# Performance work log

Measured on AMD Instinct MI355X. Metric: run time of the kernel, lower is better.

Reference implementation:

```python
import jax, jax.numpy as jnp
import numpy as np

D_MODEL = 1024
NUM_HEADS = 16
DEPTH = D_MODEL // NUM_HEADS


def setup_inputs() -> dict:
    key = jax.random.key(0)
    ks = jax.random.split(key, 8)
    B, S, D = 2, 2048, D_MODEL
    s = 1.0 / np.sqrt(D)
    return {
        "q": jax.random.normal(ks[0], (B, S, D), jnp.float32),
        "k": jax.random.normal(ks[1], (B, S, D), jnp.float32),
        "v": jax.random.normal(ks[2], (B, S, D), jnp.float32),
        "Wq": jax.random.normal(ks[3], (D, D), jnp.float32) * s,
        "bq": jnp.zeros((D,), jnp.float32),
        "Wk": jax.random.normal(ks[4], (D, D), jnp.float32) * s,
        "bk": jnp.zeros((D,), jnp.float32),
        "Wv": jax.random.normal(ks[5], (D, D), jnp.float32) * s,
        "bv": jnp.zeros((D,), jnp.float32),
        "Wo": jax.random.normal(ks[6], (D, D), jnp.float32) * s,
        "bo": jnp.zeros((D,), jnp.float32),
    }


def _split_heads(x):
    # [B,S,D] -> [B,H,S,depth]
    B, S, _ = x.shape
    return x.reshape(B, S, NUM_HEADS, DEPTH).transpose(0, 2, 1, 3)


def reference(q, k, v, Wq, bq, Wk, bk, Wv, bv, Wo, bo):
    qh = _split_heads(q @ Wq + bq)  # [B,H,S,d]
    kh = _split_heads(k @ Wk + bk)
    vh = _split_heads(v @ Wv + bv)
    scale = 1.0 / jnp.sqrt(jnp.float32(DEPTH))
    logits = jnp.einsum("bhqd,bhkd->bhqk", qh, kh) * scale  # [B,H,S,S]
    weights = jax.nn.softmax(logits, axis=-1)
    attn = jnp.einsum("bhqk,bhkd->bhqd", weights, vh)
    B, H, S, d = attn.shape
    attn = attn.transpose(0, 2, 1, 3).reshape(B, S, H * d)  # [B,S,D]
    return attn @ Wo + bo
```

## Files before the change

### kernel.cpp

```cpp
#include <hip/hip_runtime.h>
#include <hip/hip_bf16.h>
#include <stdint.h>


typedef __attribute__((ext_vector_type(8))) short bf16x8;
typedef __attribute__((ext_vector_type(4))) float f32x4;

#define MFMA16(a, b, c) __builtin_amdgcn_mfma_f32_16x16x32_bf16((a), (b), (c), 0, 0, 0)
#define EXP2(x) __builtin_amdgcn_exp2f(x)

static constexpr int S_LEN = 2048;
static constexpr int DM    = 1024;
static constexpr int DEPTH = 64;
static constexpr float QSCALE = 0.125f * 1.44269504088896340736f;

__device__ __forceinline__ unsigned short f2b(float f) {
  unsigned u = __float_as_uint(f);
  unsigned r = 0x7FFFu + ((u >> 16) & 1u);
  return (unsigned short)((u + r) >> 16);
}

__device__ __forceinline__ unsigned short b16(float f) {
  __hip_bfloat16 h = __float2bfloat16(f);
  union { __hip_bfloat16 h; unsigned short u; } c; c.h = h; return c.u;
}

__device__ __forceinline__ void gload16(const void* g, void* l) {
  __builtin_amdgcn_global_load_lds(
      (const __attribute__((address_space(1))) void*)g,
      (__attribute__((address_space(3))) void*)l, 16, 0, 0);
}

__device__ __forceinline__ void wave_lds_fence() {
  asm volatile("" ::: "memory");
  __builtin_amdgcn_sched_barrier(0);
}

__global__ __launch_bounds__(256) void prep_k(
    const float* __restrict__ xq, const float* __restrict__ xk,
    const float* __restrict__ xv, unsigned short* __restrict__ Xb,
    const float* __restrict__ Wq, const float* __restrict__ Wk,
    const float* __restrict__ Wv, const float* __restrict__ Wo,
    unsigned short* __restrict__ Wt) {
  __shared__ unsigned short ts[64][68];
  const int bid = blockIdx.x;
  const int tid = threadIdx.x;
  if (bid < 6144) {
    const int which = bid >> 11;
    const int xb = bid & 2047;
    const float* X = (which == 0) ? xq : (which == 1) ? xk : xv;
    size_t gid = ((size_t)xb * 256 + tid) * 8;
    float4 v0 = *(const float4*)&X[gid];
    float4 v1 = *(const float4*)&X[gid + 4];
    union { unsigned short u[8]; bf16x8 v; } pk;
    pk.u[0] = f2b(v0.x); pk.u[1] = f2b(v0.y); pk.u[2] = f2b(v0.z); pk.u[3] = f2b(v0.w);
    pk.u[4] = f2b(v1.x); pk.u[5] = f2b(v1.y); pk.u[6] = f2b(v1.z); pk.u[7] = f2b(v1.w);
    *(bf16x8*)&Xb[(size_t)which * 4096 * DM + gid] = pk.v;
    return;
  }
  const int wb = bid - 6144;
  const int w = wb >> 8, tile = wb & 255;
  const int tr = tile >> 4, tc = tile & 15;
  const float* W = (w == 0) ? Wq : (w == 1) ? Wk : (w == 2) ? Wv : Wo;
  unsigned short* T = Wt + (size_t)w * DM * DM;
  const int kr = tid >> 4, nc = (tid & 15) * 4;
  #pragma unroll
  for (int j = 0; j < 4; ++j) {
    int k = tr * 64 + kr + j * 16;
    float4 v = *(const float4*)&W[(size_t)k * DM + tc * 64 + nc];
    ushort4 u; u.x = f2b(v.x); u.y = f2b(v.y); u.z = f2b(v.z); u.w = f2b(v.w);
    *(ushort4*)&ts[kr + j * 16][nc] = u;
  }
  __syncthreads();
  const int nr = tid >> 4, kc = (tid & 15) * 4;
  #pragma unroll
  for (int j = 0; j < 4; ++j) {
    int n = tc * 64 + nr + j * 16;
    ushort4 u;
    u.x = ts[kc + 0][nr + j * 16];
    u.y = ts[kc + 1][nr + j * 16];
    u.z = ts[kc + 2][nr + j * 16];
    u.w = ts[kc + 3][nr + j * 16];
    *(ushort4*)&T[(size_t)n * DM + tr * 64 + kc] = u;
  }
}

__global__ __launch_bounds__(256, 4) void proj_qkv_k(
    const unsigned short* __restrict__ Xb, const unsigned short* __restrict__ Wt,
    const float* __restrict__ bq, const float* __restrict__ bk, const float* __restrict__ bv,
    unsigned short* __restrict__ Qh, unsigned short* __restrict__ Kh,
    unsigned short* __restrict__ Vt) {
  __shared__ __align__(16) unsigned short As[2][128][32];
  __shared__ __align__(16) unsigned short Bs[2][128][32];

  const int z = blockIdx.z;
  const unsigned short* A  = Xb + (size_t)z * 4096 * DM;
  const unsigned short* Bt = Wt + (size_t)z * DM * DM;
  const float* bias = (z == 0) ? bq : (z == 1) ? bk : bv;
  const float scale = (z == 0) ? QSCALE : 1.0f;
  unsigned short* O = (z == 0) ? Qh : (z == 1) ? Kh : Vt;

  const int bm = blockIdx.x, bn = blockIdx.y;
  const int tid = threadIdx.x;
  const int wave = tid >> 6, lane = tid & 63;
  const int wr = wave >> 1, wc = wave & 1;
  const int g = lane >> 4, i16 = lane & 15;
  const int srow = tid >> 2, sslot = tid & 3;

  f32x4 acc[4][4] = {};

  auto stage = [&](int ks, int buf) {
    #pragma unroll
    for (int rnd = 0; rnd < 2; ++rnd) {
      int row = rnd * 64 + srow;
      int sw = sslot ^ ((row >> 1) & 3);
      gload16(&A[(size_t)(bm * 128 + row) * DM + ks * 32 + sw * 8],
              &As[buf][row][sslot * 8]);
      gload16(&Bt[(size_t)(bn * 128 + row) * DM + ks * 32 + sw * 8],
              &Bs[buf][row][sslot * 8]);
    }
  };
  auto compute = [&](int buf) {
    bf16x8 a[4], b[4];
    #pragma unroll
    for (int m = 0; m < 4; ++m) {
      int row = wr * 64 + m * 16 + i16;
      int sl = g ^ ((row >> 1) & 3);
      a[m] = *(const bf16x8*)&As[buf][row][sl * 8];
    }
    #pragma unroll
    for (int n = 0; n < 4; ++n) {
      int row = wc * 64 + n * 16 + i16;
      int sl = g ^ ((row >> 1) & 3);
      b[n] = *(const bf16x8*)&Bs[buf][row][sl * 8];
    }
    #pragma unroll
    for (int m = 0; m < 4; ++m)
      #pragma unroll
      for (int n = 0; n < 4; ++n)
        acc[m][n] = MFMA16(a[m], b[n], acc[m][n]);
  };

  stage(0, 0);
  __syncthreads();
  int cur = 0;
  #pragma unroll 1
  for (int ks = 0; ks < DM / 32; ++ks) {
    if (ks + 1 < DM / 32) stage(ks + 1, cur ^ 1);
    compute(cur);
    __syncthreads();
    cur ^= 1;
  }

  #pragma unroll
  for (int m = 0; m < 4; ++m) {
    #pragma unroll
    for (int n = 0; n < 4; ++n) {
      #pragma unroll
      for (int r = 0; r < 4; ++r) {
        int row = bm * 128 + wr * 64 + m * 16 + g * 4 + r;
        int col = bn * 128 + wc * 64 + n * 16 + i16;
        float v = (acc[m][n][r] + bias[col]) * scale;
        int b_ = row >> 11, s = row & 2047;
        int h = col >> 6, dd = col & 63;
        if (z != 2)
          O[(((size_t)(b_ * 16 + h)) * S_LEN + s) * DEPTH + dd] = f2b(v);
        else
          O[(((size_t)(b_ * 16 + h)) * DEPTH + dd) * S_LEN + s] = f2b(v);
      }
    }
  }
}

__global__ __launch_bounds__(256, 4) void out_proj_k(
    const unsigned short* __restrict__ At, const unsigned short* __restrict__ Wto,
    const float* __restrict__ bo, float* __restrict__ out) {
  __shared__ __align__(16) unsigned short As[2][64][32];
  __shared__ __align__(16) unsigned short Bs[2][128][32];

  const int bm = blockIdx.x, bn = blockIdx.y;
  const int tid = threadIdx.x;
  const int wave = tid >> 6, lane = tid & 63;
  const int wr = wave >> 1, wc = wave & 1;
  const int g = lane >> 4, i16 = lane & 15;
  const int srow = tid >> 2, sslot = tid & 3;

  f32x4 acc[2][4] = {};

  auto stage = [&](int ks, int buf) {
    {
      int sw = sslot ^ ((srow >> 1) & 3);
      gload16(&At[(size_t)(bm * 64 + srow) * DM + ks * 32 + sw * 8],
              &As[buf][srow][sslot * 8]);
    }
    #pragma unroll
    for (int rnd = 0; rnd < 2; ++rnd) {
      int row = rnd * 64 + srow;
      int sw = sslot ^ ((row >> 1) & 3);
      gload16(&Wto[(size_t)(bn * 128 + row) * DM + ks * 32 + sw * 8],
              &Bs[buf][row][sslot * 8]);
    }
  };
  auto compute = [&](int buf) {
    bf16x8 a[2], b[4];
    #pragma unroll
    for (int m = 0; m < 2; ++m) {
      int row = wr * 32 + m * 16 + i16;
      int sl = g ^ ((row >> 1) & 3);
      a[m] = *(const bf16x8*)&As[buf][row][sl * 8];
    }
    #pragma unroll
    for (int n = 0; n < 4; ++n) {
      int row = wc * 64 + n * 16 + i16;
      int sl = g ^ ((row >> 1) & 3);
      b[n] = *(const bf16x8*)&Bs[buf][row][sl * 8];
    }
    #pragma unroll
    for (int m = 0; m < 2; ++m)
      #pragma unroll
      for (int n = 0; n < 4; ++n)
        acc[m][n] = MFMA16(a[m], b[n], acc[m][n]);
  };

  stage(0, 0);
  __syncthreads();
  int cur = 0;
  #pragma unroll 1
  for (int ks = 0; ks < DM / 32; ++ks) {
    if (ks + 1 < DM / 32) stage(ks + 1, cur ^ 1);
    compute(cur);
    __syncthreads();
    cur ^= 1;
  }

  #pragma unroll
  for (int m = 0; m < 2; ++m) {
    #pragma unroll
    for (int n = 0; n < 4; ++n) {
      #pragma unroll
      for (int r = 0; r < 4; ++r) {
        int row = bm * 64 + wr * 32 + m * 16 + g * 4 + r;
        int col = bn * 128 + wc * 64 + n * 16 + i16;
        out[(size_t)row * DM + col] = acc[m][n][r] + bo[col];
      }
    }
  }
}

__global__ __launch_bounds__(256) void attn_k(
    const unsigned short* __restrict__ Qh, const unsigned short* __restrict__ Kh,
    const unsigned short* __restrict__ Vt, unsigned short* __restrict__ Ob) {
  __shared__ unsigned short kv_lds[2][2][64][64];
  __shared__ unsigned short p_lds[4][16][64];

  const int linear = blockIdx.y * 32 + blockIdx.x;
  const int wg = (linear & 7) * 128 + (linear >> 3);
  const int qt = wg & 31, bh = wg >> 5;

  const int tid = threadIdx.x;
  const int wave = tid >> 6, lane = tid & 63;
  const int g = lane >> 4, i16 = lane & 15;

  const unsigned short* Q = Qh + (size_t)bh * S_LEN * DEPTH;
  const unsigned short* K = Kh + (size_t)bh * S_LEN * DEPTH;
  const unsigned short* V = Vt + (size_t)bh * DEPTH * S_LEN;

  const int sr0 = tid >> 3;
  const int ss0 = tid & 7;

  const int qbase = qt * 64 + wave * 16;
  const bf16x8 qa0 = *(const bf16x8*)&Q[(size_t)(qbase + i16) * DEPTH + g * 8];
  const bf16x8 qa1 = *(const bf16x8*)&Q[(size_t)(qbase + i16) * DEPTH + 32 + g * 8];

  const short one_b = (short)0x3F80;
  const bf16x8 ones = {one_b, one_b, one_b, one_b, one_b, one_b, one_b, one_b};

  f32x4 l_acc = {0.f, 0.f, 0.f, 0.f};
  f32x4 o[4] = {};

  #pragma unroll
  for (int j = 0; j < 2; ++j) {
    int r = j * 32 + sr0;
    int sw = ss0 ^ (r & 7);
    gload16(&K[(size_t)r * DEPTH + sw * 8], &kv_lds[0][0][r][ss0 * 8]);
    gload16(&V[(size_t)r * S_LEN + sw * 8], &kv_lds[0][1][r][ss0 * 8]);
  }
  __syncthreads();

  int cur = 0;
  #pragma unroll 1
  for (int t64 = 0; t64 < 32; ++t64) {
    const int kv0 = t64 * 64;
    if (t64 + 1 < 32) {
      const int nkv = kv0 + 64;
      #pragma unroll
      for (int j = 0; j < 2; ++j) {
        int r = j * 32 + sr0;
        int sw = ss0 ^ (r & 7);
        gload16(&K[(size_t)(nkv + r) * DEPTH + sw * 8], &kv_lds[cur ^ 1][0][r][ss0 * 8]);
        gload16(&V[(size_t)r * S_LEN + nkv + sw * 8],   &kv_lds[cur ^ 1][1][r][ss0 * 8]);
      }
    }

    f32x4 sT[4];
    const f32x4 zero = {0.f, 0.f, 0.f, 0.f};
    __builtin_amdgcn_s_setprio(1);
    #pragma unroll
    for (int t = 0; t < 4; ++t) {
      int row = t * 16 + i16;
      int x = row & 7;
      bf16x8 k0 = *(const bf16x8*)&kv_lds[cur][0][row][(g ^ x) * 8];
      bf16x8 k1 = *(const bf16x8*)&kv_lds[cur][0][row][((4 + g) ^ x) * 8];
      f32x4 s = MFMA16(k0, qa0, zero);
      sT[t] = MFMA16(k1, qa1, s);
    }
    __builtin_amdgcn_s_setprio(0);

    bf16x8 vf0[4], vf1[4];
    #pragma unroll
    for (int dt = 0; dt < 4; ++dt) {
      int row = dt * 16 + i16;
      int x = row & 7;
      vf0[dt] = *(const bf16x8*)&kv_lds[cur][1][row][(g ^ x) * 8];
      vf1[dt] = *(const bf16x8*)&kv_lds[cur][1][row][((4 + g) ^ x) * 8];
    }

    #pragma unroll
    for (int t = 0; t < 4; ++t) {
      ushort4 w;
      w.x = b16(EXP2(sT[t][0]));
      w.y = b16(EXP2(sT[t][1]));
      w.z = b16(EXP2(sT[t][2]));
      w.w = b16(EXP2(sT[t][3]));
      int idx = (((t * 2 + (g >> 1)) ^ (i16 & 7)) * 8) + (g & 1) * 4;
      *(ushort4*)&p_lds[wave][i16][idx] = w;
    }
    wave_lds_fence();
    bf16x8 pa0 = *(const bf16x8*)&p_lds[wave][i16][(g ^ (i16 & 7)) * 8];
    bf16x8 pa1 = *(const bf16x8*)&p_lds[wave][i16][((4 + g) ^ (i16 & 7)) * 8];

    __builtin_amdgcn_s_setprio(1);
    #pragma unroll
    for (int dt = 0; dt < 4; ++dt) {
      o[dt] = MFMA16(pa0, vf0[dt], o[dt]);
      o[dt] = MFMA16(pa1, vf1[dt], o[dt]);
    }
    l_acc = MFMA16(pa0, ones, l_acc);
    l_acc = MFMA16(pa1, ones, l_acc);
    __builtin_amdgcn_s_setprio(0);

    __syncthreads();
    cur ^= 1;
  }

  const int b_ = bh >> 4, h = bh & 15;
  f32x4 rinv;
  #pragma unroll
  for (int r = 0; r < 4; ++r)
    rinv[r] = 1.0f / l_acc[r];
  #pragma unroll
  for (int dt = 0; dt < 4; ++dt) {
    #pragma unroll
    for (int r = 0; r < 4; ++r) {
      int qrow = qbase + g * 4 + r;
      float val = o[dt][r] * rinv[r];
      Ob[((size_t)(b_ * S_LEN + qrow)) * DM + h * DEPTH + dt * 16 + i16] = f2b(val);
    }
  }
}

extern "C" void kernel_launch(void* const* d_in, const int* in_sizes, int n_in,
                              void* d_out, int out_size, void* d_ws, size_t ws_size,
                              hipStream_t stream) {
  const float* q  = (const float*)d_in[0];
  const float* k  = (const float*)d_in[1];
  const float* v  = (const float*)d_in[2];
  const float* Wq = (const float*)d_in[3];
  const float* bq = (const float*)d_in[4];
  const float* Wk = (const float*)d_in[5];
  const float* bk = (const float*)d_in[6];
  const float* Wv = (const float*)d_in[7];
  const float* bv = (const float*)d_in[8];
  const float* Wo = (const float*)d_in[9];
  const float* bo = (const float*)d_in[10];
  float* out = (float*)d_out;

  const size_t HEAD_ELEMS = (size_t)2 * 16 * S_LEN * DEPTH;
  unsigned short* Qh = (unsigned short*)d_ws;
  unsigned short* Kh = Qh + HEAD_ELEMS;
  unsigned short* Vt = Kh + HEAD_ELEMS;
  unsigned short* Xb = Vt + HEAD_ELEMS;
  unsigned short* At = Xb;
  unsigned short* Wt = Xb + 3 * HEAD_ELEMS;

  dim3 blk(256);
  hipLaunchKernelGGL(prep_k, dim3(7168), blk, 0, stream,
                     q, k, v, Xb, Wq, Wk, Wv, Wo, Wt);
  hipLaunchKernelGGL(proj_qkv_k, dim3(32, 8, 3), blk, 0, stream,
                     Xb, Wt, bq, bk, bv, Qh, Kh, Vt);
  hipLaunchKernelGGL(attn_k, dim3(32, 32), blk, 0, stream, Qh, Kh, Vt, At);
  hipLaunchKernelGGL(out_proj_k, dim3(64, 8), blk, 0, stream,
                     At, Wt + (size_t)3 * DM * DM, bo, out);
}
```

Before: 131.7 us.

## Fuse fp32-to-bf16 activation conversion into QKV projection A-tile loads

Drops the separate pass that converts q/k/v activations to bf16 in the prep kernel. The projection GEMM now reads fp32 A tiles into registers, converts them and writes them to a padded LDS buffer after compute, overlapping the global loads with MFMA work. This removes a full write-then-read round trip of the activations, at the cost of doubling A-side global traffic per tile and adding register pressure. It also unrolls the attention KV loop by two.

```diff
diff --git a/kernel.cpp b/kernel.cpp
--- a/kernel.cpp
+++ b/kernel.cpp
@@ -37,29 +37,13 @@
 }
 
 __global__ __launch_bounds__(256) void prep_k(
-    const float* __restrict__ xq, const float* __restrict__ xk,
-    const float* __restrict__ xv, unsigned short* __restrict__ Xb,
     const float* __restrict__ Wq, const float* __restrict__ Wk,
     const float* __restrict__ Wv, const float* __restrict__ Wo,
     unsigned short* __restrict__ Wt) {
   __shared__ unsigned short ts[64][68];
   const int bid = blockIdx.x;
   const int tid = threadIdx.x;
-  if (bid < 6144) {
-    const int which = bid >> 11;
-    const int xb = bid & 2047;
-    const float* X = (which == 0) ? xq : (which == 1) ? xk : xv;
-    size_t gid = ((size_t)xb * 256 + tid) * 8;
-    float4 v0 = *(const float4*)&X[gid];
-    float4 v1 = *(const float4*)&X[gid + 4];
-    union { unsigned short u[8]; bf16x8 v; } pk;
-    pk.u[0] = f2b(v0.x); pk.u[1] = f2b(v0.y); pk.u[2] = f2b(v0.z); pk.u[3] = f2b(v0.w);
-    pk.u[4] = f2b(v1.x); pk.u[5] = f2b(v1.y); pk.u[6] = f2b(v1.z); pk.u[7] = f2b(v1.w);
-    *(bf16x8*)&Xb[(size_t)which * 4096 * DM + gid] = pk.v;
-    return;
-  }
-  const int wb = bid - 6144;
-  const int w = wb >> 8, tile = wb & 255;
+  const int w = bid >> 8, tile = bid & 255;
   const int tr = tile >> 4, tc = tile & 15;
   const float* W = (w == 0) ? Wq : (w == 1) ? Wk : (w == 2) ? Wv : Wo;
   unsigned short* T = Wt + (size_t)w * DM * DM;
@@ -86,15 +70,16 @@
 }
 
 __global__ __launch_bounds__(256, 4) void proj_qkv_k(
-    const unsigned short* __restrict__ Xb, const unsigned short* __restrict__ Wt,
+    const float* __restrict__ xq, const float* __restrict__ xk,
+    const float* __restrict__ xv, const unsigned short* __restrict__ Wt,
     const float* __restrict__ bq, const float* __restrict__ bk, const float* __restrict__ bv,
     unsigned short* __restrict__ Qh, unsigned short* __restrict__ Kh,
     unsigned short* __restrict__ Vt) {
-  __shared__ __align__(16) unsigned short As[2][128][32];
+  __shared__ __align__(16) unsigned short As[2][128][40];
   __shared__ __align__(16) unsigned short Bs[2][128][32];
 
   const int z = blockIdx.z;
-  const unsigned short* A  = Xb + (size_t)z * 4096 * DM;
+  const float* A32 = (z == 0) ? xq : (z == 1) ? xk : xv;
   const unsigned short* Bt = Wt + (size_t)z * DM * DM;
   const float* bias = (z == 0) ? bq : (z == 1) ? bk : bv;
   const float scale = (z == 0) ? QSCALE : 1.0f;
@@ -106,27 +91,43 @@
   const int wr = wave >> 1, wc = wave & 1;
   const int g = lane >> 4, i16 = lane & 15;
   const int srow = tid >> 2, sslot = tid & 3;
+  const int arow = tid >> 3, ac4 = (tid & 7) * 4;
 
   f32x4 acc[4][4] = {};
-
-  auto stage = [&](int ks, int buf) {
+  float4 ah[4];
+
+  auto stageB = [&](int ks, int buf) {
     #pragma unroll
     for (int rnd = 0; rnd < 2; ++rnd) {
       int row = rnd * 64 + srow;
       int sw = sslot ^ ((row >> 1) & 3);
-      gload16(&A[(size_t)(bm * 128 + row) * DM + ks * 32 + sw * 8],
-              &As[buf][row][sslot * 8]);
       gload16(&Bt[(size_t)(bn * 128 + row) * DM + ks * 32 + sw * 8],
               &Bs[buf][row][sslot * 8]);
     }
   };
+  auto loadA = [&](int ks) {
+    #pragma unroll
+    for (int i = 0; i < 4; ++i) {
+      int row = arow + i * 32;
+      ah[i] = *(const float4*)&A32[(size_t)(bm * 128 + row) * DM + ks * 32 + ac4];
+    }
+  };
+  auto writeA = [&](int buf) {
+    #pragma unroll
+    for (int i = 0; i < 4; ++i) {
+      int row = arow + i * 32;
+      ushort4 w;
+      w.x = b16(ah[i].x); w.y = b16(ah[i].y);
+      w.z = b16(ah[i].z); w.w = b16(ah[i].w);
+      *(ushort4*)&As[buf][row][ac4] = w;
+    }
+  };
   auto compute = [&](int buf) {
     bf16x8 a[4], b[4];
     #pragma unroll
     for (int m = 0; m < 4; ++m) {
       int row = wr * 64 + m * 16 + i16;
-      int sl = g ^ ((row >> 1) & 3);
-      a[m] = *(const bf16x8*)&As[buf][row][sl * 8];
+      a[m] = *(const bf16x8*)&As[buf][row][g * 8];
     }
     #pragma unroll
     for (int n = 0; n < 4; ++n) {
@@ -141,13 +142,17 @@
         acc[m][n] = MFMA16(a[m], b[n], acc[m][n]);
   };
 
-  stage(0, 0);
+  stageB(0, 0);
+  loadA(0);
+  writeA(0);
   __syncthreads();
   int cur = 0;
   #pragma unroll 1
   for (int ks = 0; ks < DM / 32; ++ks) {
-    if (ks + 1 < DM / 32) stage(ks + 1, cur ^ 1);
+    const bool more = (ks + 1 < DM / 32);
+    if (more) { stageB(ks + 1, cur ^ 1); loadA(ks + 1); }
     compute(cur);
+    if (more) writeA(cur ^ 1);
     __syncthreads();
     cur ^= 1;
   }
@@ -288,7 +293,7 @@
   __syncthreads();
 
   int cur = 0;
-  #pragma unroll 1
+  #pragma unroll 2
   for (int t64 = 0; t64 < 32; ++t64) {
     const int kv0 = t64 * 64;
     if (t64 + 1 < 32) {
@@ -389,15 +394,13 @@
   unsigned short* Qh = (unsigned short*)d_ws;
   unsigned short* Kh = Qh + HEAD_ELEMS;
   unsigned short* Vt = Kh + HEAD_ELEMS;
-  unsigned short* Xb = Vt + HEAD_ELEMS;
-  unsigned short* At = Xb;
-  unsigned short* Wt = Xb + 3 * HEAD_ELEMS;
+  unsigned short* At = Vt + HEAD_ELEMS;
+  unsigned short* Wt = At + HEAD_ELEMS;
 
   dim3 blk(256);
-  hipLaunchKernelGGL(prep_k, dim3(7168), blk, 0, stream,
-                     q, k, v, Xb, Wq, Wk, Wv, Wo, Wt);
+  hipLaunchKernelGGL(prep_k, dim3(1024), blk, 0, stream, Wq, Wk, Wv, Wo, Wt);
   hipLaunchKernelGGL(proj_qkv_k, dim3(32, 8, 3), blk, 0, stream,
-                     Xb, Wt, bq, bk, bv, Qh, Kh, Vt);
+                     q, k, v, Wt, bq, bk, bv, Qh, Kh, Vt);
   hipLaunchKernelGGL(attn_k, dim3(32, 32), blk, 0, stream, Qh, Kh, Vt, At);
   hipLaunchKernelGGL(out_proj_k, dim3(64, 8), blk, 0, stream,
                      At, Wt + (size_t)3 * DM * DM, bo, out);
```

Result: no change. 133.4 us (+1.3%).

## Feed exp scores directly into transposed PV MFMA, dropping P LDS round-trip

Applied to the files above, without the earlier changes.

Switches the P·V product to the 16x16x16 bf16 MFMA with P as the B operand in its native S^T register layout, so exponentiated scores no longer need to be written to and reread from LDS. V fragments are read per k-slice with swizzled 8-byte LDS reads, and the row-sum uses the same instruction with a ones vector. The output becomes transposed per lane, enabling 8-byte vectorized stores. The trade-off is twice as many MFMA instructions, each half the K depth, plus more, smaller V LDS reads.

```diff
diff --git a/kernel.cpp b/kernel.cpp
--- a/kernel.cpp
+++ b/kernel.cpp
@@ -4,9 +4,11 @@
 
 
 typedef __attribute__((ext_vector_type(8))) short bf16x8;
+typedef __attribute__((ext_vector_type(4))) short bf16x4;
 typedef __attribute__((ext_vector_type(4))) float f32x4;
 
-#define MFMA16(a, b, c) __builtin_amdgcn_mfma_f32_16x16x32_bf16((a), (b), (c), 0, 0, 0)
+#define MFMA16(a, b, c)  __builtin_amdgcn_mfma_f32_16x16x32_bf16((a), (b), (c), 0, 0, 0)
+#define MFMAK16(a, b, c) __builtin_amdgcn_mfma_f32_16x16x16bf16_1k((a), (b), (c), 0, 0, 0)
 #define EXP2(x) __builtin_amdgcn_exp2f(x)
 
 static constexpr int S_LEN = 2048;
@@ -29,11 +31,6 @@
   __builtin_amdgcn_global_load_lds(
       (const __attribute__((address_space(1))) void*)g,
       (__attribute__((address_space(3))) void*)l, 16, 0, 0);
-}
-
-__device__ __forceinline__ void wave_lds_fence() {
-  asm volatile("" ::: "memory");
-  __builtin_amdgcn_sched_barrier(0);
 }
 
 __global__ __launch_bounds__(256) void prep_k(
@@ -251,7 +248,6 @@
     const unsigned short* __restrict__ Qh, const unsigned short* __restrict__ Kh,
     const unsigned short* __restrict__ Vt, unsigned short* __restrict__ Ob) {
   __shared__ unsigned short kv_lds[2][2][64][64];
-  __shared__ unsigned short p_lds[4][16][64];
 
   const int linear = blockIdx.y * 32 + blockIdx.x;
   const int wg = (linear & 7) * 128 + (linear >> 3);
@@ -273,10 +269,15 @@
   const bf16x8 qa1 = *(const bf16x8*)&Q[(size_t)(qbase + i16) * DEPTH + 32 + g * 8];
 
   const short one_b = (short)0x3F80;
-  const bf16x8 ones = {one_b, one_b, one_b, one_b, one_b, one_b, one_b, one_b};
+  const bf16x4 ones4 = {one_b, one_b, one_b, one_b};
 
   f32x4 l_acc = {0.f, 0.f, 0.f, 0.f};
   f32x4 o[4] = {};
+
+  int voff[4];
+  #pragma unroll
+  for (int t = 0; t < 4; ++t)
+    voff[t] = (i16 * 64) + (((t * 2 + (g >> 1)) ^ (i16 & 7)) * 8) + ((g & 1) * 4);
 
   #pragma unroll
   for (int j = 0; j < 2; ++j) {
@@ -316,37 +317,30 @@
     }
     __builtin_amdgcn_s_setprio(0);
 
-    bf16x8 vf0[4], vf1[4];
+    bf16x4 pb[4];
+    #pragma unroll
+    for (int t = 0; t < 4; ++t) {
+      union { unsigned short u[4]; bf16x4 v; } pk;
+      pk.u[0] = b16(EXP2(sT[t][0]));
+      pk.u[1] = b16(EXP2(sT[t][1]));
+      pk.u[2] = b16(EXP2(sT[t][2]));
+      pk.u[3] = b16(EXP2(sT[t][3]));
+      pb[t] = pk.v;
+    }
+
+    const unsigned short* vplane = &kv_lds[cur][1][0][0];
+    __builtin_amdgcn_s_setprio(1);
     #pragma unroll
     for (int dt = 0; dt < 4; ++dt) {
-      int row = dt * 16 + i16;
-      int x = row & 7;
-      vf0[dt] = *(const bf16x8*)&kv_lds[cur][1][row][(g ^ x) * 8];
-      vf1[dt] = *(const bf16x8*)&kv_lds[cur][1][row][((4 + g) ^ x) * 8];
-    }
-
-    #pragma unroll
-    for (int t = 0; t < 4; ++t) {
-      ushort4 w;
-      w.x = b16(EXP2(sT[t][0]));
-      w.y = b16(EXP2(sT[t][1]));
-      w.z = b16(EXP2(sT[t][2]));
-      w.w = b16(EXP2(sT[t][3]));
-      int idx = (((t * 2 + (g >> 1)) ^ (i16 & 7)) * 8) + (g & 1) * 4;
-      *(ushort4*)&p_lds[wave][i16][idx] = w;
-    }
-    wave_lds_fence();
-    bf16x8 pa0 = *(const bf16x8*)&p_lds[wave][i16][(g ^ (i16 & 7)) * 8];
-    bf16x8 pa1 = *(const bf16x8*)&p_lds[wave][i16][((4 + g) ^ (i16 & 7)) * 8];
-
-    __builtin_amdgcn_s_setprio(1);
-    #pragma unroll
-    for (int dt = 0; dt < 4; ++dt) {
-      o[dt] = MFMA16(pa0, vf0[dt], o[dt]);
-      o[dt] = MFMA16(pa1, vf1[dt], o[dt]);
-    }
-    l_acc = MFMA16(pa0, ones, l_acc);
-    l_acc = MFMA16(pa1, ones, l_acc);
+      #pragma unroll
+      for (int t = 0; t < 4; ++t) {
+        bf16x4 va = *(const bf16x4*)&vplane[dt * 16 * 64 + voff[t]];
+        o[dt] = MFMAK16(va, pb[t], o[dt]);
+      }
+    }
+    #pragma unroll
+    for (int t = 0; t < 4; ++t)
+      l_acc = MFMAK16(ones4, pb[t], l_acc);
     __builtin_amdgcn_s_setprio(0);
 
     __syncthreads();
@@ -354,18 +348,16 @@
   }
 
   const int b_ = bh >> 4, h = bh & 15;
-  f32x4 rinv;
-  #pragma unroll
-  for (int r = 0; r < 4; ++r)
-    rinv[r] = 1.0f / l_acc[r];
+  const float rinv = 1.0f / l_acc[0];
+  const int qrow = qbase + i16;
   #pragma unroll
   for (int dt = 0; dt < 4; ++dt) {
-    #pragma unroll
-    for (int r = 0; r < 4; ++r) {
-      int qrow = qbase + g * 4 + r;
-      float val = o[dt][r] * rinv[r];
-      Ob[((size_t)(b_ * S_LEN + qrow)) * DM + h * DEPTH + dt * 16 + i16] = f2b(val);
-    }
+    ushort4 w;
+    w.x = f2b(o[dt][0] * rinv);
+    w.y = f2b(o[dt][1] * rinv);
+    w.z = f2b(o[dt][2] * rinv);
+    w.w = f2b(o[dt][3] * rinv);
+    *(ushort4*)&Ob[((size_t)(b_ * S_LEN + qrow)) * DM + h * DEPTH + dt * 16 + g * 4] = w;
   }
 }
 
```

New measurement: 136.3 us. 3.5% more time.

## Process two 16-row query subtiles per wave in attention kernel

Applied to the files above, without the earlier changes.

Each wave now handles 32 query rows instead of 16, so a block covers 128 query rows and the grid is halved. K and V tiles loaded into LDS are reused across twice as many query rows, halving global KV traffic and LDS fragment reads per unit of work. The cost is more registers per wave (doubled accumulators and Q fragments) and fewer blocks (512), which may reduce occupancy and latency hiding.

```diff
diff --git a/kernel.cpp b/kernel.cpp
--- a/kernel.cpp
+++ b/kernel.cpp
@@ -251,11 +251,11 @@
     const unsigned short* __restrict__ Qh, const unsigned short* __restrict__ Kh,
     const unsigned short* __restrict__ Vt, unsigned short* __restrict__ Ob) {
   __shared__ unsigned short kv_lds[2][2][64][64];
-  __shared__ unsigned short p_lds[4][16][64];
-
-  const int linear = blockIdx.y * 32 + blockIdx.x;
-  const int wg = (linear & 7) * 128 + (linear >> 3);
-  const int qt = wg & 31, bh = wg >> 5;
+  __shared__ unsigned short p_lds[4][2][16][64];
+
+  const int linear = blockIdx.y * 16 + blockIdx.x;
+  const int wg = (linear & 7) * 64 + (linear >> 3);
+  const int qt = wg & 15, bh = wg >> 4;
 
   const int tid = threadIdx.x;
   const int wave = tid >> 6, lane = tid & 63;
@@ -268,15 +268,19 @@
   const int sr0 = tid >> 3;
   const int ss0 = tid & 7;
 
-  const int qbase = qt * 64 + wave * 16;
-  const bf16x8 qa0 = *(const bf16x8*)&Q[(size_t)(qbase + i16) * DEPTH + g * 8];
-  const bf16x8 qa1 = *(const bf16x8*)&Q[(size_t)(qbase + i16) * DEPTH + 32 + g * 8];
+  const int qbase = qt * 128 + wave * 32;
+  bf16x8 qa[2][2];
+  #pragma unroll
+  for (int qs = 0; qs < 2; ++qs) {
+    qa[qs][0] = *(const bf16x8*)&Q[(size_t)(qbase + qs * 16 + i16) * DEPTH + g * 8];
+    qa[qs][1] = *(const bf16x8*)&Q[(size_t)(qbase + qs * 16 + i16) * DEPTH + 32 + g * 8];
+  }
 
   const short one_b = (short)0x3F80;
   const bf16x8 ones = {one_b, one_b, one_b, one_b, one_b, one_b, one_b, one_b};
 
-  f32x4 l_acc = {0.f, 0.f, 0.f, 0.f};
-  f32x4 o[4] = {};
+  f32x4 l_acc[2] = {};
+  f32x4 o[2][4] = {};
 
   #pragma unroll
   for (int j = 0; j < 2; ++j) {
@@ -302,7 +306,7 @@
       }
     }
 
-    f32x4 sT[4];
+    f32x4 sT[2][4];
     const f32x4 zero = {0.f, 0.f, 0.f, 0.f};
     __builtin_amdgcn_s_setprio(1);
     #pragma unroll
@@ -311,42 +315,53 @@
       int x = row & 7;
       bf16x8 k0 = *(const bf16x8*)&kv_lds[cur][0][row][(g ^ x) * 8];
       bf16x8 k1 = *(const bf16x8*)&kv_lds[cur][0][row][((4 + g) ^ x) * 8];
-      f32x4 s = MFMA16(k0, qa0, zero);
-      sT[t] = MFMA16(k1, qa1, s);
+      #pragma unroll
+      for (int qs = 0; qs < 2; ++qs) {
+        f32x4 s = MFMA16(k0, qa[qs][0], zero);
+        sT[qs][t] = MFMA16(k1, qa[qs][1], s);
+      }
     }
     __builtin_amdgcn_s_setprio(0);
 
-    bf16x8 vf0[4], vf1[4];
+    #pragma unroll
+    for (int qs = 0; qs < 2; ++qs) {
+      #pragma unroll
+      for (int t = 0; t < 4; ++t) {
+        ushort4 w;
+        w.x = b16(EXP2(sT[qs][t][0]));
+        w.y = b16(EXP2(sT[qs][t][1]));
+        w.z = b16(EXP2(sT[qs][t][2]));
+        w.w = b16(EXP2(sT[qs][t][3]));
+        int idx = (((t * 2 + (g >> 1)) ^ (i16 & 7)) * 8) + (g & 1) * 4;
+        *(ushort4*)&p_lds[wave][qs][i16][idx] = w;
+      }
+    }
+    wave_lds_fence();
+    bf16x8 pa0[2], pa1[2];
+    #pragma unroll
+    for (int qs = 0; qs < 2; ++qs) {
+      pa0[qs] = *(const bf16x8*)&p_lds[wave][qs][i16][(g ^ (i16 & 7)) * 8];
+      pa1[qs] = *(const bf16x8*)&p_lds[wave][qs][i16][((4 + g) ^ (i16 & 7)) * 8];
+    }
+
+    __builtin_amdgcn_s_setprio(1);
     #pragma unroll
     for (int dt = 0; dt < 4; ++dt) {
       int row = dt * 16 + i16;
       int x = row & 7;
-      vf0[dt] = *(const bf16x8*)&kv_lds[cur][1][row][(g ^ x) * 8];
-      vf1[dt] = *(const bf16x8*)&kv_lds[cur][1][row][((4 + g) ^ x) * 8];
-    }
-
-    #pragma unroll
-    for (int t = 0; t < 4; ++t) {
-      ushort4 w;
-      w.x = b16(EXP2(sT[t][0]));
-      w.y = b16(EXP2(sT[t][1]));
-      w.z = b16(EXP2(sT[t][2]));
-      w.w = b16(EXP2(sT[t][3]));
-      int idx = (((t * 2 + (g >> 1)) ^ (i16 & 7)) * 8) + (g & 1) * 4;
-      *(ushort4*)&p_lds[wave][i16][idx] = w;
-    }
-    wave_lds_fence();
-    bf16x8 pa0 = *(const bf16x8*)&p_lds[wave][i16][(g ^ (i16 & 7)) * 8];
-    bf16x8 pa1 = *(const bf16x8*)&p_lds[wave][i16][((4 + g) ^ (i16 & 7)) * 8];
-
-    __builtin_amdgcn_s_setprio(1);
-    #pragma unroll
-    for (int dt = 0; dt < 4; ++dt) {
-      o[dt] = MFMA16(pa0, vf0[dt], o[dt]);
-      o[dt] = MFMA16(pa1, vf1[dt], o[dt]);
-    }
-    l_acc = MFMA16(pa0, ones, l_acc);
-    l_acc = MFMA16(pa1, ones, l_acc);
+      bf16x8 v0 = *(const bf16x8*)&kv_lds[cur][1][row][(g ^ x) * 8];
+      bf16x8 v1 = *(const bf16x8*)&kv_lds[cur][1][row][((4 + g) ^ x) * 8];
+      #pragma unroll
+      for (int qs = 0; qs < 2; ++qs) {
+        o[qs][dt] = MFMA16(pa0[qs], v0, o[qs][dt]);
+        o[qs][dt] = MFMA16(pa1[qs], v1, o[qs][dt]);
+      }
+    }
+    #pragma unroll
+    for (int qs = 0; qs < 2; ++qs) {
+      l_acc[qs] = MFMA16(pa0[qs], ones, l_acc[qs]);
+      l_acc[qs] = MFMA16(pa1[qs], ones, l_acc[qs]);
+    }
     __builtin_amdgcn_s_setprio(0);
 
     __syncthreads();
@@ -354,17 +369,20 @@
   }
 
   const int b_ = bh >> 4, h = bh & 15;
-  f32x4 rinv;
-  #pragma unroll
-  for (int r = 0; r < 4; ++r)
-    rinv[r] = 1.0f / l_acc[r];
-  #pragma unroll
-  for (int dt = 0; dt < 4; ++dt) {
-    #pragma unroll
-    for (int r = 0; r < 4; ++r) {
-      int qrow = qbase + g * 4 + r;
-      float val = o[dt][r] * rinv[r];
-      Ob[((size_t)(b_ * S_LEN + qrow)) * DM + h * DEPTH + dt * 16 + i16] = f2b(val);
+  #pragma unroll
+  for (int qs = 0; qs < 2; ++qs) {
+    f32x4 rinv;
+    #pragma unroll
+    for (int r = 0; r < 4; ++r)
+      rinv[r] = 1.0f / l_acc[qs][r];
+    #pragma unroll
+    for (int dt = 0; dt < 4; ++dt) {
+      #pragma unroll
+      for (int r = 0; r < 4; ++r) {
+        int qrow = qbase + qs * 16 + g * 4 + r;
+        float val = o[qs][dt][r] * rinv[r];
+        Ob[((size_t)(b_ * S_LEN + qrow)) * DM + h * DEPTH + dt * 16 + i16] = f2b(val);
+      }
     }
   }
 }
@@ -398,7 +416,7 @@
                      q, k, v, Xb, Wq, Wk, Wv, Wo, Wt);
   hipLaunchKernelGGL(proj_qkv_k, dim3(32, 8, 3), blk, 0, stream,
                      Xb, Wt, bq, bk, bv, Qh, Kh, Vt);
-  hipLaunchKernelGGL(attn_k, dim3(32, 32), blk, 0, stream, Qh, Kh, Vt, At);
+  hipLaunchKernelGGL(attn_k, dim3(16, 32), blk, 0, stream, Qh, Kh, Vt, At);
   hipLaunchKernelGGL(out_proj_k, dim3(64, 8), blk, 0, stream,
                      At, Wt + (size_t)3 * DM * DM, bo, out);
 }
```

Measured after the change: 124.5 us. 5.4% less time.
